# Performance work log

Hardware: AMD Instinct MI355X
Metric: run time of the kernel (lower is better)

The kernel has to match this reference:

```python
import jax, jax.numpy as jnp
import numpy as np


def _pick(key, nodes, mask, cnt):
    # Uniformly pick one of the `cnt` entries of `nodes` where mask is True.
    r = jax.random.randint(key, (), 0, jnp.maximum(cnt, 1))
    cs = jnp.cumsum(mask.astype(jnp.int32))
    return nodes[jnp.argmax(cs == r + 1)]


def _one_walk(key, nbrs, f0, n_faces, L):
    # nbrs: [N,3] int32 neighbor table, f0: scalar start face.
    seq = jnp.zeros((L + 1,), jnp.int32).at[0].set(f0)
    visited = jnp.zeros((n_faces + 1,), bool).at[n_faces].set(True).at[f0].set(True)

    def cond(st):
        return st[2] <= L

    def body(st):
        seq, visited, i, bs, k = st
        k, k1, k2, k3 = jax.random.split(k, 4)
        cur = seq[i - 1]
        nb = nbrs[cur]                     # [3] neighbor candidates
        unv = ~visited[nb]
        cnt = unv.sum()
        need = cnt == 0                    # stuck -> backtrack
        cand = _pick(k1, nb, unv, cnt)

        def bcond(c):
            bs_c, found = c[0], c[1]
            return need & (~found) & (i > bs_c)

        def bbody(c):
            bs_c, found, ta, kk = c
            kk, kp = jax.random.split(kk)
            back = seq[i - bs_c - 1]
            bn = nbrs[back]
            bm = ~visited[bn]
            bc = bm.sum()
            f2 = bc > 0
            ta2 = _pick(kp, bn, bm, bc)
            return (jnp.where(f2, bs_c, bs_c + 2), f2, jnp.where(f2, ta2, ta), kk)

        bs_f, found, ta_bt, _ = jax.lax.while_loop(
            bcond, bbody, (bs, jnp.array(False), jnp.int32(0), k2))
        rand_node = jax.random.randint(k3, (), 0, n_faces, dtype=jnp.int32)
        to_add = jnp.where(~need, cand, jnp.where(found, ta_bt, rand_node))
        hit = need & found                 # successful backtrack
        bs_new = jnp.where(hit, bs_f, jnp.int32(1))
        i_new = jnp.where(hit, i - bs_f, i)
        ar = jnp.arange(L + 1, dtype=jnp.int32)
        # torch: replace seq[i-bs:i] with to_add on successful backtrack
        seq = jnp.where(hit & (ar >= i_new) & (ar < i), to_add, seq)
        visited = visited.at[to_add].set(True)
        seq = seq.at[i_new].set(to_add)
        return (seq, visited, i_new + 1, bs_new, k)

    seq, *_ = jax.lax.while_loop(
        cond, body, (seq, visited, jnp.int32(1), jnp.int32(1), key))
    return seq


def patch_random_walk(key, neighbors, centers, n_faces, seq_len):
    B, G = centers.shape
    keys = jax.random.split(key, B * G).reshape(B, G)
    walk_g = jax.vmap(_one_walk, in_axes=(0, None, 0, None, None))
    walk_bg = jax.vmap(walk_g, in_axes=(0, 0, 0, None, None))
    return walk_bg(keys, neighbors, centers, n_faces, seq_len)  # [B,G,L+1] int32


def setup_inputs() -> dict:
    key = jax.random.key(0)
    k1, k2, k3 = jax.random.split(key, 3)
    B, N, G = 4, 20000, 1024
    xyz = jax.random.normal(k1, (B, N, 3), dtype=jnp.float32)
    neighbors = jax.random.randint(k2, (B, N, 3), 0, N, dtype=jnp.int32)
    centers = jax.random.randint(k3, (B, G), 0, N, dtype=jnp.int32)
    return {"xyz": xyz, "neighbors": neighbors, "centers": centers,
            "n_faces": N, "seq_len": 63}


def reference(xyz, neighbors, centers, n_faces, seq_len):
    # patch_random_walk -> idx [B,G,K]; then Group.forward gather + recenter.
    idx = patch_random_walk(jax.random.key(42), neighbors, centers, n_faces, seq_len)
    gather = jax.vmap(lambda p, i: p[i])(xyz, idx)            # [B,G,K,3]
    center_xyz = jax.vmap(lambda p, c: p[c])(xyz, centers)    # [B,G,3]
    return gather - center_xyz[:, :, None, :]
```

## Files before the change

### kernel.cpp

```cpp
#include <hip/hip_runtime.h>
#include <stdint.h>
#include <stddef.h>


namespace {

__device__ __forceinline__ uint32_t rotl32(uint32_t x, int r) {
  return (x << r) | (x >> (32 - r));
}

__device__ __forceinline__ void tf2x32(uint32_t ka, uint32_t kb,
                                       uint32_t x0, uint32_t x1,
                                       uint32_t& o0, uint32_t& o1) {
  const uint32_t kc = ka ^ kb ^ 0x1BD11BDAu;
  x0 += ka; x1 += kb;
#define TF_R4(r0, r1, r2, r3)                          \
  x0 += x1; x1 = rotl32(x1, r0); x1 ^= x0;             \
  x0 += x1; x1 = rotl32(x1, r1); x1 ^= x0;             \
  x0 += x1; x1 = rotl32(x1, r2); x1 ^= x0;             \
  x0 += x1; x1 = rotl32(x1, r3); x1 ^= x0;
  TF_R4(13, 15, 26, 6)  x0 += kb; x1 += kc + 1u;
  TF_R4(17, 29, 16, 24) x0 += kc; x1 += ka + 2u;
  TF_R4(13, 15, 26, 6)  x0 += ka; x1 += kb + 3u;
  TF_R4(17, 29, 16, 24) x0 += kb; x1 += kc + 4u;
  TF_R4(13, 15, 26, 6)  x0 += kc; x1 += ka + 5u;
#undef TF_R4
  o0 = x0; o1 = x1;
}

__device__ __forceinline__ void randbits(uint32_t ka, uint32_t kb,
                                         uint32_t& hi, uint32_t& lo) {
  uint32_t s0a, s0b, s1a, s1b, h0, h1;
  tf2x32(ka, kb, 0u, 0u, s0a, s0b);
  tf2x32(ka, kb, 0u, 1u, s1a, s1b);
  tf2x32(s0a, s0b, 0u, 0u, h0, h1);
  hi = h0 ^ h1;
  tf2x32(s1a, s1b, 0u, 0u, h0, h1);
  lo = h0 ^ h1;
}

__device__ __forceinline__ uint32_t r_generic(uint32_t hi, uint32_t lo,
                                              uint32_t span) {
  uint32_t mult = 65536u % span;
  mult = (mult * mult) % span;
  return ((hi % span) * mult + (lo % span)) % span;
}

__device__ __forceinline__ uint32_t pick_code(uint32_t hi, uint32_t lo) {
  return ((hi % 3u + lo % 3u) % 3u) | ((lo & 1u) << 2);
}

__device__ __noinline__ void live_key(int w, int idx, uint32_t& ka,
                                      uint32_t& kb) {
  tf2x32(0u, 42u, 0u, (uint32_t)w, ka, kb);
  for (int c = 0; c < idx; ++c) tf2x32(ka, kb, 0u, 0u, ka, kb);
}

constexpr int CH = 64;
constexpr int WPB = 16;
constexpr int BMW = 626;
constexpr int NMAX = BMW * 32;
constexpr int SEQS = 66;
constexpr int KSTRIDE = 65;
constexpr int VISW = 2048;

__global__ __launch_bounds__(256) void walk_fast(
    const float* __restrict__ xyz, const int* __restrict__ nbrs,
    const int* __restrict__ centers, const int* __restrict__ n_faces_p,
    const int* __restrict__ seq_len_p, float* __restrict__ out,
    int s0, int num_walks, int Lp1) {
  __shared__ uint32_t nb01L[NMAX];
  __shared__ uint16_t nb2L[NMAX];
  __shared__ uint32_t visL[WPB * BMW];
  __shared__ uint16_t seqL[WPB * SEQS];
  __shared__ uint8_t  codesL[WPB * CH];

  const int tid = threadIdx.x, lane = tid & 63;
  const int w0 = blockIdx.x * WPB;
  if (w0 >= num_walks) return;
  const int N = *n_faces_p, L = *seq_len_p;
  const int B = s0 / (3 * N), G = num_walks / B;
  const bool fast = (N <= NMAX) && (L <= 63) && (G % WPB == 0);
  if (!fast) return;

  const int b = w0 / G;
  const int* __restrict__ nbs  = nbrs + (size_t)b * N * 3;
  const float* __restrict__ xb = xyz + (size_t)b * N * 3;

  if (tid < 64) {
    if (lane < WPB && (w0 + lane) < num_walks) {
      uint32_t ka, kb;
      tf2x32(0u, 42u, 0u, (uint32_t)(w0 + lane), ka, kb);
      visL[(lane * CH + 0) * 2 + 0] = ka;
      visL[(lane * CH + 0) * 2 + 1] = kb;
#pragma clang loop unroll(disable)
      for (int c = 1; c < CH; ++c) {
        tf2x32(ka, kb, 0u, 0u, ka, kb);
        visL[(lane * CH + c) * 2 + 0] = ka;
        visL[(lane * CH + c) * 2 + 1] = kb;
      }
    }
  } else {
    for (int r = tid - 64; r < N; r += 192) {
      const int3 v = *reinterpret_cast<const int3*>(nbs + 3 * (size_t)r);
      nb01L[r] = (uint32_t)v.x | ((uint32_t)v.y << 16);
      nb2L[r]  = (uint16_t)v.z;
    }
  }
  __syncthreads();

  for (int t = 0; t < 4; ++t) {
    const int g = tid * 4 + t;
    const int wl = g >> 6;
    if ((w0 + wl) < num_walks) {
      const uint32_t ka = visL[g * 2 + 0], kb = visL[g * 2 + 1];
      uint32_t k1a, k1b, hi, lo;
      tf2x32(ka, kb, 0u, 1u, k1a, k1b);
      randbits(k1a, k1b, hi, lo);
      codesL[g] = (uint8_t)pick_code(hi, lo);
    }
  }
  __syncthreads();

  for (int j = tid; j < WPB * BMW; j += 256) visL[j] = 0u;
  __syncthreads();

  if (tid < 64) {
    const int wl = lane;
    const int wg = w0 + wl;
    const bool alive = (wl < WPB) && (wg < num_walks);

    int f0 = 0, n0 = 0, n1 = 0, n2 = 0, i = 1, bs = 1, cstep = 0;
    if (alive) {
      f0 = centers[wg];
      seqL[wl * SEQS + 0] = (uint16_t)f0;
      visL[wl * BMW + ((unsigned)f0 >> 5)] = 1u << (f0 & 31);
      const uint32_t p = nb01L[f0];
      n0 = (int)(p & 0xffffu); n1 = (int)(p >> 16); n2 = (int)nb2L[f0];
    }
    for (;;) {
      const bool go = alive && (i <= L);
      if (!__ballot(go)) break;
      if (go) {
        const int idx = cstep; ++cstep;
        const uint32_t wa = visL[wl * BMW + ((unsigned)n0 >> 5)];
        const uint32_t wb = visL[wl * BMW + ((unsigned)n1 >> 5)];
        const uint32_t wc = visL[wl * BMW + ((unsigned)n2 >> 5)];
        const uint32_t pA = nb01L[n0]; const uint32_t a2 = nb2L[n0];
        const uint32_t pB = nb01L[n1]; const uint32_t b2 = nb2L[n1];
        const uint32_t pC = nb01L[n2]; const uint32_t c2 = nb2L[n2];
        const uint32_t u0 = ((wa >> (n0 & 31)) & 1u) ^ 1u;
        const uint32_t u1 = ((wb >> (n1 & 31)) & 1u) ^ 1u;
        const uint32_t u2 = ((wc >> (n2 & 31)) & 1u) ^ 1u;
        const uint32_t cnt = u0 + u1 + u2;

        int to_add, sel;
        if (__builtin_expect(cnt == 0, 0)) {
          sel = -1;
          uint32_t kia, kib;
          live_key(wg, idx, kia, kib);
          uint32_t kka, kkb;
          tf2x32(kia, kib, 0u, 2u, kka, kkb);
          bool found = false;
          int ta = 0, bsc = bs;
          while (!found && i > bsc) {
            uint32_t ca, cb, kpa, kpb;
            tf2x32(kka, kkb, 0u, 0u, ca, cb);
            tf2x32(kka, kkb, 0u, 1u, kpa, kpb);
            const int back = (int)seqL[wl * SEQS + (i - bsc - 1)];
            const uint32_t pm = nb01L[back];
            const int m0 = (int)(pm & 0xffffu), m1 = (int)(pm >> 16);
            const int m2 = (int)nb2L[back];
            const uint32_t e0 =
                ((visL[wl * BMW + (m0 >> 5)] >> (m0 & 31)) & 1u) ^ 1u;
            const uint32_t e1 =
                ((visL[wl * BMW + (m1 >> 5)] >> (m1 & 31)) & 1u) ^ 1u;
            const uint32_t e2 =
                ((visL[wl * BMW + (m2 >> 5)] >> (m2 & 31)) & 1u) ^ 1u;
            const uint32_t bc = e0 + e1 + e2;
            if (bc > 0) {
              uint32_t bhi, blo;
              randbits(kpa, kpb, bhi, blo);
              const uint32_t bcode = pick_code(bhi, blo);
              const uint32_t r3 = bcode & 3u, r2 = (bcode >> 2) & 1u;
              const uint32_t t2v = (bc == 3 ? r3 : (bc == 2 ? r2 : 0)) + 1;
              ta = (e0 == t2v) ? m0 : ((e0 + e1 == t2v) ? m1 : m2);
              found = true;
            } else {
              bsc += 2;
            }
            kka = ca; kkb = cb;
          }
          if (found) {
            const int i_new = i - bsc;
            for (int a = i_new; a < i; ++a)
              seqL[wl * SEQS + a] = (uint16_t)ta;
            to_add = ta; bs = bsc; i = i_new;
          } else {
            uint32_t k3a, k3b, rh, rl;
            tf2x32(kia, kib, 0u, 3u, k3a, k3b);
            randbits(k3a, k3b, rh, rl);
            to_add = (int)r_generic(rh, rl, (uint32_t)N);
            bs = 1;
          }
        } else {
          uint32_t code;
          if (__builtin_expect(idx >= CH, 0)) {
            uint32_t ia, ib, k1a, k1b, h2, l2;
            live_key(wg, idx, ia, ib);
            tf2x32(ia, ib, 0u, 1u, k1a, k1b);
            randbits(k1a, k1b, h2, l2);
            code = pick_code(h2, l2);
          } else {
            code = codesL[(wl << 6) | idx];
          }
          const uint32_t r3 = code & 3u, r2 = (code >> 2) & 1u;
          const uint32_t target = (cnt == 3 ? r3 : (cnt == 2 ? r2 : 0)) + 1;
          sel = (u0 == target) ? 0 : ((u0 + u1 == target) ? 1 : 2);
          to_add = (sel == 0) ? n0 : ((sel == 1) ? n1 : n2);
          bs = 1;
        }
        const unsigned word = wl * BMW + ((unsigned)to_add >> 5);
        visL[word] = visL[word] | (1u << (to_add & 31));
        seqL[wl * SEQS + i] = (uint16_t)to_add;
        ++i;
        if (sel == 0)      { n0 = (int)(pA & 0xffffu); n1 = (int)(pA >> 16); n2 = (int)a2; }
        else if (sel == 1) { n0 = (int)(pB & 0xffffu); n1 = (int)(pB >> 16); n2 = (int)b2; }
        else if (sel == 2) { n0 = (int)(pC & 0xffffu); n1 = (int)(pC >> 16); n2 = (int)c2; }
        else {
          const uint32_t p = nb01L[to_add];
          n0 = (int)(p & 0xffffu); n1 = (int)(p >> 16); n2 = (int)nb2L[to_add];
        }
      }
    }
  }
  __syncthreads();

  for (int idx = tid; idx < WPB * Lp1; idx += 256) {
    const int wl = idx / Lp1, t = idx - wl * Lp1;
    const int wg = w0 + wl;
    if (wg < num_walks) {
      const int node = (int)seqL[wl * SEQS + t];
      const int c0 = centers[wg];
      float3 v;
      v.x = xb[3 * (size_t)node + 0] - xb[3 * (size_t)c0 + 0];
      v.y = xb[3 * (size_t)node + 1] - xb[3 * (size_t)c0 + 1];
      v.z = xb[3 * (size_t)node + 2] - xb[3 * (size_t)c0 + 2];
      *reinterpret_cast<float3*>(out + ((size_t)wg * Lp1 + t) * 3) = v;
    }
  }
}

__global__ __launch_bounds__(1024) void walk_any(
    const float* __restrict__ xyz, const int* __restrict__ nbrs,
    const int* __restrict__ centers, const int* __restrict__ n_faces_p,
    const int* __restrict__ seq_len_p, float* __restrict__ out,
    int s0, int num_walks, int Lp1) {
  __shared__ uint32_t visL[WPB * VISW];
  __shared__ uint2 keysL[WPB * KSTRIDE];

  const int tid = threadIdx.x;
  const int wv = tid >> 6, lane = tid & 63;
  const int w0 = blockIdx.x * WPB;
  if (w0 >= num_walks) return;
  const int N = *n_faces_p, L = *seq_len_p;
  const int B = s0 / (3 * N), G = num_walks / B;
  if ((N <= NMAX) && (L <= 63) && (G % WPB == 0)) return;
  const int w = w0 + wv;
  const bool active = (w < num_walks);
  const bool bm_ok = (N <= VISW * 32);

  const int bb = (active ? w : w0) / G;
  const int* __restrict__ nb   = nbrs + (size_t)bb * N * 3;
  const float* __restrict__ xb = xyz + (size_t)bb * N * 3;

  const int f0 = active ? centers[w] : 0;
  int3 row = active ? *reinterpret_cast<const int3*>(nb + 3 * (size_t)f0)
                    : make_int3(0, 0, 0);

  uint32_t* __restrict__ visW = visL + wv * VISW;
  if (bm_ok) {
    for (int j = lane; j < VISW; j += 64) visW[j] = 0u;
    if (lane == 0 && active) visW[(unsigned)f0 >> 5] = 1u << (f0 & 31);
  }
  if (wv == 0 && lane < WPB && (w0 + lane) < num_walks) {
    uint32_t ka, kb;
    tf2x32(0u, 42u, 0u, (uint32_t)(w0 + lane), ka, kb);
    keysL[lane * KSTRIDE + 0] = make_uint2(ka, kb);
#pragma clang loop unroll(disable)
    for (int c2 = 1; c2 < CH; ++c2) {
      tf2x32(ka, kb, 0u, 0u, ka, kb);
      keysL[lane * KSTRIDE + c2] = make_uint2(ka, kb);
    }
  }
  __syncthreads();
  if (!active) return;

  const uint2 mykey = keysL[wv * KSTRIDE + lane];
  uint32_t mycode;
  {
    uint32_t k1a, k1b, hi, lo;
    tf2x32(mykey.x, mykey.y, 0u, 1u, k1a, k1b);
    randbits(k1a, k1b, hi, lo);
    mycode = pick_code(hi, lo);
  }
  uint32_t extka = 0, extkb = 0;
  int extc = -1;
  auto get_key = [&](int idx, uint32_t& ra, uint32_t& rb) {
    if (idx < CH) {
      ra = (uint32_t)__shfl((int)mykey.x, idx);
      rb = (uint32_t)__shfl((int)mykey.y, idx);
    } else {
      if (extc < 0) {
        extka = (uint32_t)__shfl((int)mykey.x, CH - 1);
        extkb = (uint32_t)__shfl((int)mykey.y, CH - 1);
        extc = CH - 1;
      }
      while (extc < idx) { tf2x32(extka, extkb, 0u, 0u, extka, extkb); ++extc; }
      ra = extka; rb = extkb;
    }
  };

  int seqr = (lane == 0) ? f0 : -1;
  int i = 1, bs = 1, c = 0;
  int hist = (lane == 0) ? f0 : -1, hist2 = -1;

  while (i <= L) {
    const int idx = c; ++c;
    const bool deep = (idx >= CH);
    const int n0 = row.x, n1 = row.y, n2 = row.z;
    uint32_t u0, u1, u2;
    if (bm_ok) {
      u0 = ((visW[(unsigned)n0 >> 5] >> (n0 & 31)) & 1u) ^ 1u;
      u1 = ((visW[(unsigned)n1 >> 5] >> (n1 & 31)) & 1u) ^ 1u;
      u2 = ((visW[(unsigned)n2 >> 5] >> (n2 & 31)) & 1u) ^ 1u;
    } else {
      int v0 = __any(hist == n0), v1 = __any(hist == n1), v2 = __any(hist == n2);
      if (deep) {
        v0 |= __any(hist2 == n0); v1 |= __any(hist2 == n1); v2 |= __any(hist2 == n2);
      }
      u0 = 1 - v0; u1 = 1 - v1; u2 = 1 - v2;
    }
    const uint32_t cnt = u0 + u1 + u2;

    int to_add;
    bool hit = false;
    int bsf = bs;
    if (cnt > 0) {
      uint32_t code;
      if (deep) {
        uint32_t ia, ib, k1a, k1b, hi, lo;
        get_key(idx, ia, ib);
        tf2x32(ia, ib, 0u, 1u, k1a, k1b);
        randbits(k1a, k1b, hi, lo);
        code = pick_code(hi, lo);
      } else {
        code = (uint32_t)__builtin_amdgcn_readlane((int)mycode, idx);
      }
      const uint32_t r3 = code & 3u, r2 = (code >> 2) & 1u;
      const uint32_t target = (cnt == 3 ? r3 : (cnt == 2 ? r2 : 0)) + 1;
      to_add = (u0 == target) ? n0 : ((u0 + u1 == target) ? n1 : n2);
    } else {
      uint32_t kia, kib;
      get_key(idx, kia, kib);
      uint32_t kka, kkb;
      tf2x32(kia, kib, 0u, 2u, kka, kkb);
      bool found = false;
      int ta = 0, bsc = bs;
      while (!found && i > bsc) {
        uint32_t ca, cb, kpa, kpb;
        tf2x32(kka, kkb, 0u, 0u, ca, cb);
        tf2x32(kka, kkb, 0u, 1u, kpa, kpb);
        const int back = __shfl(seqr, i - bsc - 1);
        const int3 br = *reinterpret_cast<const int3*>(nb + 3 * (size_t)back);
        uint32_t e0, e1, e2;
        if (bm_ok) {
          e0 = ((visW[(unsigned)br.x >> 5] >> (br.x & 31)) & 1u) ^ 1u;
          e1 = ((visW[(unsigned)br.y >> 5] >> (br.y & 31)) & 1u) ^ 1u;
          e2 = ((visW[(unsigned)br.z >> 5] >> (br.z & 31)) & 1u) ^ 1u;
        } else {
          int a0 = __any(hist == br.x), a1 = __any(hist == br.y), a2m = __any(hist == br.z);
          if (deep) {
            a0 |= __any(hist2 == br.x); a1 |= __any(hist2 == br.y); a2m |= __any(hist2 == br.z);
          }
          e0 = 1 - a0; e1 = 1 - a1; e2 = 1 - a2m;
        }
        const uint32_t bc = e0 + e1 + e2;
        if (bc > 0) {
          uint32_t bhi, blo;
          randbits(kpa, kpb, bhi, blo);
          const uint32_t bcode = pick_code(bhi, blo);
          const uint32_t r3 = bcode & 3u, r2 = (bcode >> 2) & 1u;
          const uint32_t t2v = (bc == 3 ? r3 : (bc == 2 ? r2 : 0)) + 1;
          ta = (e0 == t2v) ? br.x : ((e0 + e1 == t2v) ? br.y : br.z);
          found = true;
        } else {
          bsc += 2;
        }
        kka = ca; kkb = cb;
      }
      if (found) {
        to_add = ta; hit = true; bsf = bsc;
      } else {
        uint32_t k3a, k3b, rh, rl;
        tf2x32(kia, kib, 0u, 3u, k3a, k3b);
        randbits(k3a, k3b, rh, rl);
        to_add = (int)r_generic(rh, rl, (uint32_t)N);
      }
    }

    int i_new, up;
    if (hit) { i_new = i - bsf; bs = bsf; up = i - 1; }
    else     { i_new = i;       bs = 1;   up = i; }
    seqr = (lane >= i_new && lane <= up) ? to_add : seqr;
    if (bm_ok) {
      if (lane == 0) {
        const unsigned word = (unsigned)to_add >> 5;
        visW[word] |= 1u << (to_add & 31);
      }
    } else {
      const int slot = idx + 1;
      if (slot < CH)          hist  = (lane == slot)      ? to_add : hist;
      else if (slot < 2 * CH) hist2 = (lane == slot - CH) ? to_add : hist2;
    }
    i = i_new + 1;
    row = *reinterpret_cast<const int3*>(nb + 3 * (size_t)to_add);
  }

  const float cx = xb[3 * (size_t)f0 + 0];
  const float cy = xb[3 * (size_t)f0 + 1];
  const float cz = xb[3 * (size_t)f0 + 2];
  if (lane < Lp1) {
    const int node = seqr;
    float3 v;
    v.x = xb[3 * (size_t)node + 0] - cx;
    v.y = xb[3 * (size_t)node + 1] - cy;
    v.z = xb[3 * (size_t)node + 2] - cz;
    *reinterpret_cast<float3*>(out + ((size_t)w * Lp1 + lane) * 3) = v;
  }
}

}

extern "C" void kernel_launch(void* const* d_in, const int* in_sizes, int n_in,
                              void* d_out, int out_size, void* d_ws, size_t ws_size,
                              hipStream_t stream) {
  const float* xyz     = (const float*)d_in[0];
  const int*   nbrs    = (const int*)d_in[1];
  const int*   centers = (const int*)d_in[2];
  const int*   n_faces = (const int*)d_in[3];
  const int*   seq_len = (const int*)d_in[4];
  float* out = (float*)d_out;

  const int s0 = in_sizes[0];
  const int num_walks = in_sizes[2];
  const int Lp1 = out_size / (3 * num_walks);

  const int blocks = (num_walks + WPB - 1) / WPB;
  walk_fast<<<blocks, 256, 0, stream>>>(
      xyz, nbrs, centers, n_faces, seq_len, out, s0, num_walks, Lp1);
  walk_any<<<blocks, WPB * 64, 0, stream>>>(
      xyz, nbrs, centers, n_faces, seq_len, out, s0, num_walks, Lp1);
}
```

Measured before the change: 103.8 us.

## Overlap random-key generation with walk via flag-polled shared codes in larger blocks

Block size grows to 1024 threads. The neighbor-table load is spread across all threads, and the separate key-precompute, code and clear phases are removed. Fifteen helper wavefronts now generate the per-step pick codes while wavefront 0 runs the walks, publishing each code with a high-bit ready flag. The walking wave spin-polls volatile shared memory until the flag is set. This is meant to take the serial threefry chain off the critical path before the walk starts. The risks are spin-wait contention, lower occupancy from the larger block, and shared arrays sized exactly to N=20000, which no longer leaves padding.

```diff
diff --git a/kernel.cpp b/kernel.cpp
--- a/kernel.cpp
+++ b/kernel.cpp
@@ -58,83 +58,60 @@
 
 constexpr int CH = 64;
 constexpr int WPB = 16;
-constexpr int BMW = 626;
-constexpr int NMAX = BMW * 32;
-constexpr int SEQS = 66;
+constexpr int NMAXF = 20000;
+constexpr int BMWF = 625;
+constexpr int SEQSF = 64;
+constexpr int NTHR = 1024;
 constexpr int KSTRIDE = 65;
 constexpr int VISW = 2048;
-
-__global__ __launch_bounds__(256) void walk_fast(
+constexpr int NMAX = 20032;
+
+__global__ __launch_bounds__(NTHR) void walk_fast(
     const float* __restrict__ xyz, const int* __restrict__ nbrs,
     const int* __restrict__ centers, const int* __restrict__ n_faces_p,
     const int* __restrict__ seq_len_p, float* __restrict__ out,
     int s0, int num_walks, int Lp1) {
-  __shared__ uint32_t nb01L[NMAX];
-  __shared__ uint16_t nb2L[NMAX];
-  __shared__ uint32_t visL[WPB * BMW];
-  __shared__ uint16_t seqL[WPB * SEQS];
+  __shared__ uint32_t nb01L[NMAXF];
+  __shared__ uint16_t nb2L[NMAXF];
+  __shared__ uint32_t visL[WPB * BMWF];
+  __shared__ uint16_t seqL[WPB * SEQSF];
   __shared__ uint8_t  codesL[WPB * CH];
 
-  const int tid = threadIdx.x, lane = tid & 63;
+  const int tid = threadIdx.x, lane = tid & 63, wv = tid >> 6;
   const int w0 = blockIdx.x * WPB;
   if (w0 >= num_walks) return;
   const int N = *n_faces_p, L = *seq_len_p;
   const int B = s0 / (3 * N), G = num_walks / B;
-  const bool fast = (N <= NMAX) && (L <= 63) && (G % WPB == 0);
+  const bool fast = (N <= NMAXF) && (L <= 63) && (G % WPB == 0);
   if (!fast) return;
 
   const int b = w0 / G;
   const int* __restrict__ nbs  = nbrs + (size_t)b * N * 3;
   const float* __restrict__ xb = xyz + (size_t)b * N * 3;
 
-  if (tid < 64) {
-    if (lane < WPB && (w0 + lane) < num_walks) {
-      uint32_t ka, kb;
-      tf2x32(0u, 42u, 0u, (uint32_t)(w0 + lane), ka, kb);
-      visL[(lane * CH + 0) * 2 + 0] = ka;
-      visL[(lane * CH + 0) * 2 + 1] = kb;
-#pragma clang loop unroll(disable)
-      for (int c = 1; c < CH; ++c) {
-        tf2x32(ka, kb, 0u, 0u, ka, kb);
-        visL[(lane * CH + c) * 2 + 0] = ka;
-        visL[(lane * CH + c) * 2 + 1] = kb;
-      }
-    }
-  } else {
-    for (int r = tid - 64; r < N; r += 192) {
-      const int3 v = *reinterpret_cast<const int3*>(nbs + 3 * (size_t)r);
-      nb01L[r] = (uint32_t)v.x | ((uint32_t)v.y << 16);
-      nb2L[r]  = (uint16_t)v.z;
-    }
-  }
+  int f0 = 0;
+  const bool walk_lane = (wv == 0) && (lane < WPB) && (w0 + lane < num_walks);
+  if (walk_lane) f0 = centers[w0 + lane];
+
+  for (int r = tid; r < N; r += NTHR) {
+    const int3 v = *reinterpret_cast<const int3*>(nbs + 3 * (size_t)r);
+    nb01L[r] = (uint32_t)v.x | ((uint32_t)v.y << 16);
+    nb2L[r]  = (uint16_t)v.z;
+  }
+  for (int j = tid; j < WPB * BMWF; j += NTHR) visL[j] = 0u;
+  codesL[tid < WPB * CH ? tid : 0] = 0u;
   __syncthreads();
 
-  for (int t = 0; t < 4; ++t) {
-    const int g = tid * 4 + t;
-    const int wl = g >> 6;
-    if ((w0 + wl) < num_walks) {
-      const uint32_t ka = visL[g * 2 + 0], kb = visL[g * 2 + 1];
-      uint32_t k1a, k1b, hi, lo;
-      tf2x32(ka, kb, 0u, 1u, k1a, k1b);
-      randbits(k1a, k1b, hi, lo);
-      codesL[g] = (uint8_t)pick_code(hi, lo);
-    }
-  }
-  __syncthreads();
-
-  for (int j = tid; j < WPB * BMW; j += 256) visL[j] = 0u;
-  __syncthreads();
-
-  if (tid < 64) {
+  if (wv == 0) {
     const int wl = lane;
     const int wg = w0 + wl;
-    const bool alive = (wl < WPB) && (wg < num_walks);
-
-    int f0 = 0, n0 = 0, n1 = 0, n2 = 0, i = 1, bs = 1, cstep = 0;
+    const bool alive = walk_lane;
+    volatile uint8_t* __restrict__ codesV = codesL;
+
+    int n0 = 0, n1 = 0, n2 = 0, i = 1, bs = 1, cstep = 0;
     if (alive) {
-      f0 = centers[wg];
-      seqL[wl * SEQS + 0] = (uint16_t)f0;
-      visL[wl * BMW + ((unsigned)f0 >> 5)] = 1u << (f0 & 31);
+      seqL[wl * SEQSF + 0] = (uint16_t)f0;
+      visL[wl * BMWF + ((unsigned)f0 >> 5)] = 1u << (f0 & 31);
       const uint32_t p = nb01L[f0];
       n0 = (int)(p & 0xffffu); n1 = (int)(p >> 16); n2 = (int)nb2L[f0];
     }
@@ -143,9 +120,9 @@
       if (!__ballot(go)) break;
       if (go) {
         const int idx = cstep; ++cstep;
-        const uint32_t wa = visL[wl * BMW + ((unsigned)n0 >> 5)];
-        const uint32_t wb = visL[wl * BMW + ((unsigned)n1 >> 5)];
-        const uint32_t wc = visL[wl * BMW + ((unsigned)n2 >> 5)];
+        const uint32_t wa = visL[wl * BMWF + ((unsigned)n0 >> 5)];
+        const uint32_t wb = visL[wl * BMWF + ((unsigned)n1 >> 5)];
+        const uint32_t wc = visL[wl * BMWF + ((unsigned)n2 >> 5)];
         const uint32_t pA = nb01L[n0]; const uint32_t a2 = nb2L[n0];
         const uint32_t pB = nb01L[n1]; const uint32_t b2 = nb2L[n1];
         const uint32_t pC = nb01L[n2]; const uint32_t c2 = nb2L[n2];
@@ -167,16 +144,16 @@
             uint32_t ca, cb, kpa, kpb;
             tf2x32(kka, kkb, 0u, 0u, ca, cb);
             tf2x32(kka, kkb, 0u, 1u, kpa, kpb);
-            const int back = (int)seqL[wl * SEQS + (i - bsc - 1)];
+            const int back = (int)seqL[wl * SEQSF + (i - bsc - 1)];
             const uint32_t pm = nb01L[back];
             const int m0 = (int)(pm & 0xffffu), m1 = (int)(pm >> 16);
             const int m2 = (int)nb2L[back];
             const uint32_t e0 =
-                ((visL[wl * BMW + (m0 >> 5)] >> (m0 & 31)) & 1u) ^ 1u;
+                ((visL[wl * BMWF + (m0 >> 5)] >> (m0 & 31)) & 1u) ^ 1u;
             const uint32_t e1 =
-                ((visL[wl * BMW + (m1 >> 5)] >> (m1 & 31)) & 1u) ^ 1u;
+                ((visL[wl * BMWF + (m1 >> 5)] >> (m1 & 31)) & 1u) ^ 1u;
             const uint32_t e2 =
-                ((visL[wl * BMW + (m2 >> 5)] >> (m2 & 31)) & 1u) ^ 1u;
+                ((visL[wl * BMWF + (m2 >> 5)] >> (m2 & 31)) & 1u) ^ 1u;
             const uint32_t bc = e0 + e1 + e2;
             if (bc > 0) {
               uint32_t bhi, blo;
@@ -194,7 +171,7 @@
           if (found) {
             const int i_new = i - bsc;
             for (int a = i_new; a < i; ++a)
-              seqL[wl * SEQS + a] = (uint16_t)ta;
+              seqL[wl * SEQSF + a] = (uint16_t)ta;
             to_add = ta; bs = bsc; i = i_new;
           } else {
             uint32_t k3a, k3b, rh, rl;
@@ -212,7 +189,9 @@
             randbits(k1a, k1b, h2, l2);
             code = pick_code(h2, l2);
           } else {
-            code = codesL[(wl << 6) | idx];
+            uint8_t bv = codesV[(wl << 6) | idx];
+            while (!(bv & 0x80u)) bv = codesV[(wl << 6) | idx];
+            code = bv & 0x7fu;
           }
           const uint32_t r3 = code & 3u, r2 = (code >> 2) & 1u;
           const uint32_t target = (cnt == 3 ? r3 : (cnt == 2 ? r2 : 0)) + 1;
@@ -220,9 +199,9 @@
           to_add = (sel == 0) ? n0 : ((sel == 1) ? n1 : n2);
           bs = 1;
         }
-        const unsigned word = wl * BMW + ((unsigned)to_add >> 5);
+        const unsigned word = wl * BMWF + ((unsigned)to_add >> 5);
         visL[word] = visL[word] | (1u << (to_add & 31));
-        seqL[wl * SEQS + i] = (uint16_t)to_add;
+        seqL[wl * SEQSF + i] = (uint16_t)to_add;
         ++i;
         if (sel == 0)      { n0 = (int)(pA & 0xffffu); n1 = (int)(pA >> 16); n2 = (int)a2; }
         else if (sel == 1) { n0 = (int)(pB & 0xffffu); n1 = (int)(pB >> 16); n2 = (int)b2; }
@@ -233,14 +212,31 @@
         }
       }
     }
+  } else {
+    if (lane < WPB) {
+      const int wg = w0 + lane;
+      uint32_t ka, kb;
+      tf2x32(0u, 42u, 0u, (uint32_t)wg, ka, kb);
+      const int phase = wv - 1;
+#pragma clang loop unroll(disable)
+      for (int c2 = 0; c2 < CH; ++c2) {
+        if (c2 % 15 == phase) {
+          uint32_t k1a, k1b, hi, lo;
+          tf2x32(ka, kb, 0u, 1u, k1a, k1b);
+          randbits(k1a, k1b, hi, lo);
+          codesL[(lane << 6) | c2] = (uint8_t)(pick_code(hi, lo) | 0x80u);
+        }
+        tf2x32(ka, kb, 0u, 0u, ka, kb);
+      }
+    }
   }
   __syncthreads();
 
-  for (int idx = tid; idx < WPB * Lp1; idx += 256) {
+  for (int idx = tid; idx < WPB * Lp1; idx += NTHR) {
     const int wl = idx / Lp1, t = idx - wl * Lp1;
     const int wg = w0 + wl;
     if (wg < num_walks) {
-      const int node = (int)seqL[wl * SEQS + t];
+      const int node = (int)seqL[wl * SEQSF + t];
       const int c0 = centers[wg];
       float3 v;
       v.x = xb[3 * (size_t)node + 0] - xb[3 * (size_t)c0 + 0];
@@ -265,7 +261,7 @@
   if (w0 >= num_walks) return;
   const int N = *n_faces_p, L = *seq_len_p;
   const int B = s0 / (3 * N), G = num_walks / B;
-  if ((N <= NMAX) && (L <= 63) && (G % WPB == 0)) return;
+  if ((N <= NMAXF) && (L <= 63) && (G % WPB == 0)) return;
   const int w = w0 + wv;
   const bool active = (w < num_walks);
   const bool bm_ok = (N <= VISW * 32);
@@ -457,7 +453,7 @@
   const int Lp1 = out_size / (3 * num_walks);
 
   const int blocks = (num_walks + WPB - 1) / WPB;
-  walk_fast<<<blocks, 256, 0, stream>>>(
+  walk_fast<<<blocks, NTHR, 0, stream>>>(
       xyz, nbrs, centers, n_faces, seq_len, out, s0, num_walks, Lp1);
   walk_any<<<blocks, WPB * 64, 0, stream>>>(
       xyz, nbrs, centers, n_faces, seq_len, out, s0, num_walks, Lp1);
```

After: 120.0 us. +15.6%, slower.
